# Performance work log

Hardware: AMD Instinct MI355X
Metric: run time of the kernel (lower is better)

Reference implementation:

```python
import jax, jax.numpy as jnp
import numpy as np

B, T, D, U = 16, 8192, 256, 256


def setup_inputs() -> dict:
    key = jax.random.key(0)
    k1, k2, k3, k4, k5 = jax.random.split(key, 5)
    scale = 1.0 / np.sqrt(D)
    return {
        "query": jax.random.normal(k1, (B, D), dtype=jnp.float32),
        "value": jax.random.normal(k2, (B, T, D), dtype=jnp.float32),
        "W1": jax.random.normal(k3, (D, U), dtype=jnp.float32) * scale,
        "W2": jax.random.normal(k4, (D, U), dtype=jnp.float32) * scale,
        "V": jax.random.normal(k5, (U, 1), dtype=jnp.float32) * scale,
    }


def reference(query, value, W1, W2, V):
    # query: [B, D], value: [B, T, D]
    # additive (Bahdanau) attention:
    #   score_t = V^T tanh(W1 value_t + W2 query)
    hidden = jnp.einsum('bd,du->bu', query, W2)[:, None, :]       # [B, 1, U]
    keys = jnp.einsum('btd,du->btu', value, W1)                   # [B, T, U]
    score = jnp.einsum('btu,uo->bto', jnp.tanh(keys + hidden), V) # [B, T, 1]
    attention_weights = jax.nn.softmax(score, axis=1)             # over time
    context_vector = jnp.sum(attention_weights * value, axis=1)   # [B, D]
    return context_vector
```

## Files before the change

### kernel.cpp

```cpp
#include <hip/hip_runtime.h>
#include <cstdint>
#include <cstddef>

#define B_ 16
#define T_ 8192
#define D_ 256
#define U_ 256

typedef __attribute__((ext_vector_type(8))) short bf16x8;
typedef __attribute__((ext_vector_type(4))) float f32x4;
typedef __attribute__((ext_vector_type(4))) unsigned int u32x4;

#define VMCNT(N) asm volatile("s_waitcnt vmcnt(" #N ")" ::: "memory")
#define SBAR()   asm volatile("s_barrier" ::: "memory")
#define FENCE()  asm volatile("" ::: "memory")

__device__ inline f32x4 mfma16(bf16x8 a, bf16x8 b, f32x4 c) {
    return __builtin_amdgcn_mfma_f32_16x16x32_bf16(a, b, c, 0, 0, 0);
}

__device__ inline unsigned int pack2_hi(float x, float y) {
    return __builtin_amdgcn_perm(__float_as_uint(y), __float_as_uint(x), 0x07060302u);
}
__device__ inline float lo_part(float x) {
    return x - __uint_as_float(__float_as_uint(x) & 0xffff0000u);
}

__device__ inline void cvt8v(const float4 a, const float4 b, bf16x8& hi, bf16x8& lo) {
    u32x4 h, l;
    h[0] = pack2_hi(a.x, a.y);
    h[1] = pack2_hi(a.z, a.w);
    h[2] = pack2_hi(b.x, b.y);
    h[3] = pack2_hi(b.z, b.w);
    l[0] = pack2_hi(lo_part(a.x), lo_part(a.y));
    l[1] = pack2_hi(lo_part(a.z), lo_part(a.w));
    l[2] = pack2_hi(lo_part(b.x), lo_part(b.y));
    l[3] = pack2_hi(lo_part(b.z), lo_part(b.w));
    hi = __builtin_bit_cast(bf16x8, h);
    lo = __builtin_bit_cast(bf16x8, l);
}

__global__ __launch_bounds__(256) void prep_w1t_kernel(const float* __restrict__ W1,
                                                       unsigned short* __restrict__ hi,
                                                       unsigned short* __restrict__ lo) {
    const int idx = blockIdx.x * 256 + threadIdx.x;
    const int d = idx >> 8;
    const int u = idx & 255;
    const float x = W1[idx];
    const unsigned int xb = __float_as_uint(x);
    const unsigned short h = (unsigned short)(xb >> 16);
    const float lf = x - __uint_as_float(xb & 0xffff0000u);
    const unsigned short lo16 = (unsigned short)(__float_as_uint(lf) >> 16);
    hi[u * D_ + d] = h;
    lo[u * D_ + d] = lo16;
}

__global__ __launch_bounds__(256) void hidden_kernel(const float* __restrict__ q,
                                                     const float* __restrict__ W2,
                                                     float* __restrict__ hidden) {
    const int b = blockIdx.x;
    const int u = threadIdx.x;
    __shared__ float qs[D_];
    qs[u] = q[b * D_ + u];
    __syncthreads();
    float acc = 0.f;
#pragma unroll 8
    for (int d = 0; d < D_; ++d)
        acc += qs[d] * W2[d * U_ + u];
    hidden[b * U_ + u] = acc;
}

__global__ __launch_bounds__(256, 2) void scores_ctx_kernel(
        const float* __restrict__ value,
        const unsigned short* __restrict__ w1t_hi,
        const unsigned short* __restrict__ w1t_lo,
        const float* __restrict__ Vv,
        const float* __restrict__ hidden,
        float* __restrict__ partial,
        float* __restrict__ mstat,
        float* __restrict__ lstat) {
    const int b    = blockIdx.y;
    const int bx   = blockIdx.x;
    const int t0   = bx * 128;
    const int tid  = threadIdx.x;
    const int w    = tid >> 6;
    const int lane = tid & 63;
    const int lr   = lane & 15;
    const int lk   = lane >> 4;

    __shared__ unsigned short bhi[2][16 * 512];
    __shared__ unsigned short blo[2][16 * 512];
    __shared__ float s_lds[128];
    __shared__ float e_lds[128];
    __shared__ float redm[4];
    __shared__ float redl[4];

    auto stage_b = [&](int bf, int k0) {
#pragma unroll
        for (int i = 0; i < 4; ++i) {
            const int uf = w * 4 + i;
            const unsigned short* gh = w1t_hi + (size_t)(uf * 16 + lr) * D_ + k0 + lk * 8;
            __builtin_amdgcn_global_load_lds(
                (const __attribute__((address_space(1))) void*)gh,
                (__attribute__((address_space(3))) void*)&bhi[bf][uf * 512],
                16, 0, 0);
            const unsigned short* gl = w1t_lo + (size_t)(uf * 16 + lr) * D_ + k0 + lk * 8;
            __builtin_amdgcn_global_load_lds(
                (const __attribute__((address_space(1))) void*)gl,
                (__attribute__((address_space(3))) void*)&blo[bf][uf * 512],
                16, 0, 0);
        }
    };

    f32x4 acc[2][16] = {};
    const float* aptr = value + ((size_t)b * T_ + t0 + w * 32 + lr) * D_ + lk * 8;

    stage_b(0, 0);
    float4 a0[2], a1[2];
#pragma unroll
    for (int tf = 0; tf < 2; ++tf) {
        a0[tf] = *reinterpret_cast<const float4*>(aptr + (size_t)tf * 16 * D_);
        a1[tf] = *reinterpret_cast<const float4*>(aptr + (size_t)tf * 16 * D_ + 4);
    }
    FENCE();
    VMCNT(4);
    SBAR();

    int cur = 0;
    for (int k = 0; k < 8; ++k) {
        const int k0 = k << 5;

        float4 n0[2], n1[2];
        if (k < 7) {
            stage_b(cur ^ 1, k0 + 32);
#pragma unroll
            for (int tf = 0; tf < 2; ++tf) {
                n0[tf] = *reinterpret_cast<const float4*>(aptr + (size_t)tf * 16 * D_ + k0 + 32);
                n1[tf] = *reinterpret_cast<const float4*>(aptr + (size_t)tf * 16 * D_ + k0 + 36);
            }
        }
        FENCE();

        bf16x8 ah[2], al[2];
#pragma unroll
        for (int tf = 0; tf < 2; ++tf)
            cvt8v(a0[tf], a1[tf], ah[tf], al[tf]);

#pragma unroll
        for (int uf = 0; uf < 16; ++uf) {
            const bf16x8 bh = *reinterpret_cast<const bf16x8*>(&bhi[cur][uf * 512 + lane * 8]);
            const bf16x8 bl = *reinterpret_cast<const bf16x8*>(&blo[cur][uf * 512 + lane * 8]);
#pragma unroll
            for (int tf = 0; tf < 2; ++tf) {
                acc[tf][uf] = mfma16(ah[tf], bh, acc[tf][uf]);
                acc[tf][uf] = mfma16(al[tf], bh, acc[tf][uf]);
                acc[tf][uf] = mfma16(ah[tf], bl, acc[tf][uf]);
            }
        }

        if (k < 7) {
            VMCNT(4);
            SBAR();
#pragma unroll
            for (int tf = 0; tf < 2; ++tf) { a0[tf] = n0[tf]; a1[tf] = n1[tf]; }
        }
        cur ^= 1;
    }

    float hv[16], vwv[16];
#pragma unroll
    for (int uf = 0; uf < 16; ++uf) {
        const int u = uf * 16 + lr;
        hv[uf]  = hidden[b * U_ + u];
        vwv[uf] = Vv[u];
    }
#pragma unroll
    for (int tf = 0; tf < 2; ++tf) {
#pragma unroll
        for (int r = 0; r < 4; ++r) {
            float p = 0.f;
#pragma unroll
            for (int uf = 0; uf < 16; ++uf) {
                const float z = acc[tf][uf][r] + hv[uf];
                const float e = __expf(2.f * z);
                p += (1.f - __fdividef(2.f, e + 1.f)) * vwv[uf];
            }
            p += __shfl_xor(p, 1, 64);
            p += __shfl_xor(p, 2, 64);
            p += __shfl_xor(p, 4, 64);
            p += __shfl_xor(p, 8, 64);
            if (lr == 0) s_lds[w * 32 + tf * 16 + lk * 4 + r] = p;
        }
    }
    __syncthreads();

    float x = (tid < 128) ? s_lds[tid] : -3e38f;
#pragma unroll
    for (int m = 1; m < 64; m <<= 1) x = fmaxf(x, __shfl_xor(x, m, 64));
    if (lane == 0) redm[w] = x;
    __syncthreads();
    const float mc = fmaxf(fmaxf(redm[0], redm[1]), fmaxf(redm[2], redm[3]));

    float e = 0.f;
    if (tid < 128) {
        e = __expf(s_lds[tid] - mc);
        e_lds[tid] = e;
    }
    float l = e;
#pragma unroll
    for (int m = 1; m < 64; m <<= 1) l += __shfl_xor(l, m, 64);
    if (lane == 0) redl[w] = l;
    __syncthreads();
    const float lc = redl[0] + redl[1] + redl[2] + redl[3];

    const float* vb = value + ((size_t)b * T_ + t0) * D_ + tid;
    float ca0 = 0.f, ca1 = 0.f;
#pragma unroll 8
    for (int t = 0; t < 128; t += 2) {
        ca0 += e_lds[t]     * vb[(size_t)t * D_];
        ca1 += e_lds[t + 1] * vb[(size_t)(t + 1) * D_];
    }
    partial[((size_t)b * 64 + bx) * D_ + tid] = ca0 + ca1;
    if (tid == 0) {
        mstat[b * 64 + bx] = mc;
        lstat[b * 64 + bx] = lc;
    }
}

__global__ __launch_bounds__(256) void combine_kernel(const float* __restrict__ partial,
                                                      const float* __restrict__ mstat,
                                                      const float* __restrict__ lstat,
                                                      float* __restrict__ out) {
    const int b = blockIdx.x;
    const int d = threadIdx.x;
    float M = -3e38f;
#pragma unroll 8
    for (int c = 0; c < 64; ++c) M = fmaxf(M, mstat[b * 64 + c]);
    float L = 0.f, a = 0.f;
#pragma unroll 4
    for (int c = 0; c < 64; ++c) {
        const float s = __expf(mstat[b * 64 + c] - M);
        L += lstat[b * 64 + c] * s;
        a += s * partial[((size_t)b * 64 + c) * D_ + d];
    }
    out[b * D_ + d] = a / L;
}

extern "C" void kernel_launch(void* const* d_in, const int* in_sizes, int n_in,
                              void* d_out, int out_size, void* d_ws, size_t ws_size,
                              hipStream_t stream) {
    const float* q     = (const float*)d_in[0];
    const float* value = (const float*)d_in[1];
    const float* W1    = (const float*)d_in[2];
    const float* W2    = (const float*)d_in[3];
    const float* Vv    = (const float*)d_in[4];
    float* out = (float*)d_out;

    char* ws = (char*)d_ws;
    unsigned short* w1t_hi  = (unsigned short*)(ws);
    unsigned short* w1t_lo  = (unsigned short*)(ws + 131072);
    float*          hidden  = (float*)(ws + 262144);
    float*          partial = (float*)(ws + 278528);
    float*          mstat   = (float*)(ws + 1327104);
    float*          lstat   = (float*)(ws + 1331200);

    prep_w1t_kernel<<<dim3(256), dim3(256), 0, stream>>>(W1, w1t_hi, w1t_lo);
    hidden_kernel<<<dim3(B_), dim3(256), 0, stream>>>(q, W2, hidden);

    dim3 g2(T_ / 128, B_);
    scores_ctx_kernel<<<g2, dim3(256), 0, stream>>>(value, w1t_hi, w1t_lo, Vv, hidden,
                                                    partial, mstat, lstat);

    combine_kernel<<<dim3(B_), dim3(256), 0, stream>>>(partial, mstat, lstat, out);
}
```

Measured before the change: 106.7 us.

## Split W1 staging into two U-halves to halve LDS buffer footprint

The W1 hi/lo LDS staging buffers are halved by splitting the U dimension into two 128-wide halves. Each k-step now stages one half while computing on the other, and the separate next-A prefetch registers are dropped. The aim is to cut LDS use and register pressure so more blocks fit per CU. In exchange there are more barriers and a full vmcnt(0) wait inside each k-step, which serialises loads with compute.

```diff
diff --git a/kernel.cpp b/kernel.cpp
--- a/kernel.cpp
+++ b/kernel.cpp
@@ -88,26 +88,28 @@
     const int lr   = lane & 15;
     const int lk   = lane >> 4;
 
-    __shared__ unsigned short bhi[2][16 * 512];
-    __shared__ unsigned short blo[2][16 * 512];
+    __shared__ unsigned short bhi[2][8 * 512];
+    __shared__ unsigned short blo[2][8 * 512];
     __shared__ float s_lds[128];
     __shared__ float e_lds[128];
     __shared__ float redm[4];
     __shared__ float redl[4];
 
-    auto stage_b = [&](int bf, int k0) {
-#pragma unroll
-        for (int i = 0; i < 4; ++i) {
-            const int uf = w * 4 + i;
-            const unsigned short* gh = w1t_hi + (size_t)(uf * 16 + lr) * D_ + k0 + lk * 8;
+    auto stage_b = [&](int bf, int uh, int k0) {
+#pragma unroll
+        for (int i = 0; i < 2; ++i) {
+            const int ufl = w * 2 + i;
+            const unsigned short* gh =
+                w1t_hi + (size_t)(uh * 128 + ufl * 16 + lr) * D_ + k0 + lk * 8;
             __builtin_amdgcn_global_load_lds(
                 (const __attribute__((address_space(1))) void*)gh,
-                (__attribute__((address_space(3))) void*)&bhi[bf][uf * 512],
+                (__attribute__((address_space(3))) void*)&bhi[bf][ufl * 512],
                 16, 0, 0);
-            const unsigned short* gl = w1t_lo + (size_t)(uf * 16 + lr) * D_ + k0 + lk * 8;
+            const unsigned short* gl =
+                w1t_lo + (size_t)(uh * 128 + ufl * 16 + lr) * D_ + k0 + lk * 8;
             __builtin_amdgcn_global_load_lds(
                 (const __attribute__((address_space(1))) void*)gl,
-                (__attribute__((address_space(3))) void*)&blo[bf][uf * 512],
+                (__attribute__((address_space(3))) void*)&blo[bf][ufl * 512],
                 16, 0, 0);
         }
     };
@@ -115,7 +117,7 @@
     f32x4 acc[2][16] = {};
     const float* aptr = value + ((size_t)b * T_ + t0 + w * 32 + lr) * D_ + lk * 8;
 
-    stage_b(0, 0);
+    stage_b(0, 0, 0);
     float4 a0[2], a1[2];
 #pragma unroll
     for (int tf = 0; tf < 2; ++tf) {
@@ -126,45 +128,53 @@
     VMCNT(4);
     SBAR();
 
-    int cur = 0;
     for (int k = 0; k < 8; ++k) {
         const int k0 = k << 5;
 
-        float4 n0[2], n1[2];
-        if (k < 7) {
-            stage_b(cur ^ 1, k0 + 32);
-#pragma unroll
-            for (int tf = 0; tf < 2; ++tf) {
-                n0[tf] = *reinterpret_cast<const float4*>(aptr + (size_t)tf * 16 * D_ + k0 + 32);
-                n1[tf] = *reinterpret_cast<const float4*>(aptr + (size_t)tf * 16 * D_ + k0 + 36);
-            }
-        }
-        FENCE();
-
         bf16x8 ah[2], al[2];
 #pragma unroll
         for (int tf = 0; tf < 2; ++tf)
             cvt8v(a0[tf], a1[tf], ah[tf], al[tf]);
-
-#pragma unroll
-        for (int uf = 0; uf < 16; ++uf) {
-            const bf16x8 bh = *reinterpret_cast<const bf16x8*>(&bhi[cur][uf * 512 + lane * 8]);
-            const bf16x8 bl = *reinterpret_cast<const bf16x8*>(&blo[cur][uf * 512 + lane * 8]);
+        stage_b(1, 1, k0);
+        FENCE();
+#pragma unroll
+        for (int ufl = 0; ufl < 8; ++ufl) {
+            const bf16x8 bh = *reinterpret_cast<const bf16x8*>(&bhi[0][ufl * 512 + lane * 8]);
+            const bf16x8 bl = *reinterpret_cast<const bf16x8*>(&blo[0][ufl * 512 + lane * 8]);
 #pragma unroll
             for (int tf = 0; tf < 2; ++tf) {
-                acc[tf][uf] = mfma16(ah[tf], bh, acc[tf][uf]);
-                acc[tf][uf] = mfma16(al[tf], bh, acc[tf][uf]);
-                acc[tf][uf] = mfma16(ah[tf], bl, acc[tf][uf]);
-            }
-        }
-
+                acc[tf][ufl] = mfma16(ah[tf], bh, acc[tf][ufl]);
+                acc[tf][ufl] = mfma16(al[tf], bh, acc[tf][ufl]);
+                acc[tf][ufl] = mfma16(ah[tf], bl, acc[tf][ufl]);
+            }
+        }
+        VMCNT(0);
+        SBAR();
+
+        if (k < 7) {
+            stage_b(0, 0, k0 + 32);
+#pragma unroll
+            for (int tf = 0; tf < 2; ++tf) {
+                a0[tf] = *reinterpret_cast<const float4*>(aptr + (size_t)tf * 16 * D_ + k0 + 32);
+                a1[tf] = *reinterpret_cast<const float4*>(aptr + (size_t)tf * 16 * D_ + k0 + 36);
+            }
+            FENCE();
+        }
+#pragma unroll
+        for (int ufl = 0; ufl < 8; ++ufl) {
+            const bf16x8 bh = *reinterpret_cast<const bf16x8*>(&bhi[1][ufl * 512 + lane * 8]);
+            const bf16x8 bl = *reinterpret_cast<const bf16x8*>(&blo[1][ufl * 512 + lane * 8]);
+#pragma unroll
+            for (int tf = 0; tf < 2; ++tf) {
+                acc[tf][8 + ufl] = mfma16(ah[tf], bh, acc[tf][8 + ufl]);
+                acc[tf][8 + ufl] = mfma16(al[tf], bh, acc[tf][8 + ufl]);
+                acc[tf][8 + ufl] = mfma16(ah[tf], bl, acc[tf][8 + ufl]);
+            }
+        }
         if (k < 7) {
             VMCNT(4);
             SBAR();
-#pragma unroll
-            for (int tf = 0; tf < 2; ++tf) { a0[tf] = n0[tf]; a1[tf] = n1[tf]; }
-        }
-        cur ^= 1;
+        }
     }
 
     float hv[16], vwv[16];
```

New measurement: 107.4 us. No clear change (+0.7%).
